# Kernel tuning notes

Measured on AMD Instinct MI355X. Metric: run time of the kernel, lower is better.

Reference implementation:

```python
import jax, jax.numpy as jnp
import numpy as np

N = 50000       # nodes
D_IN = 256      # in_channels
D_OUT = 256     # out_channels
E1 = 300000     # edges for TAGConv branch
E2 = 300000     # edges for attention branch


def setup_inputs() -> dict:
    key = jax.random.key(0)
    ks = jax.random.split(key, 8)
    s = 1.0 / np.sqrt(D_IN)  # torch Linear default init range
    u = lambda k: jax.random.uniform(k, (D_IN, D_OUT), jnp.float32, -s, s)
    return {
        "x": jax.random.normal(ks[0], (N, D_IN), jnp.float32),
        "edge_index": jax.random.randint(ks[1], (2, E1), 0, N),
        "edge_index_2": jax.random.randint(ks[2], (2, E2), 0, N),
        "W0": u(ks[3]),  # TAGConv hop-0 weight
        "W1": u(ks[4]),  # TAGConv hop-1 weight
        "Wq": u(ks[5]),  # attention query proj
        "Wk": u(ks[6]),  # attention key proj
        "Wv": u(ks[7]),  # attention value proj
    }


def reference(x, edge_index, edge_index_2, W0, W1, Wq, Wk, Wv):
    # --- TAGConv branch: K=1, normalize=False, bias=False ---
    src, dst = edge_index[0], edge_index[1]
    agg = jax.ops.segment_sum(x[src], dst, num_segments=N)   # A @ x, [N, D_IN]
    x1 = x @ W0 + agg @ W1                                   # [N, D_OUT]

    # --- Transformer_Block branch over edge_index_2, use_softmax=False ---
    q = x @ Wq
    k = x @ Wk
    v = x @ Wv
    s2, d2 = edge_index_2[0], edge_index_2[1]
    attn = jnp.einsum('ed,ed->e', q[d2], k[s2])              # per-edge raw score
    x2 = jax.ops.segment_sum(attn[:, None] * v[s2], d2, num_segments=N)

    return x1 - x2
```

## Files before the change

### kernel.cpp

```cpp
#include <hip/hip_runtime.h>

#define TD 256

typedef __attribute__((ext_vector_type(8))) short short8;
typedef __attribute__((ext_vector_type(8))) unsigned short ushort8;
typedef __attribute__((ext_vector_type(4))) float f32x4;

__device__ inline unsigned short f2bf(float f) {
  unsigned u = __float_as_uint(f);
  u = u + 0x7fffu + ((u >> 16) & 1u);
  return (unsigned short)(u >> 16);
}
__device__ inline float bf2f(unsigned short h) {
  return __uint_as_float(((unsigned)h) << 16);
}

__global__ __launch_bounds__(256) void prologue_kernel(
    const int* __restrict__ ei, int E1, const int* __restrict__ ei2, int E2,
    int* __restrict__ deg1, int* __restrict__ deg2,
    const float* __restrict__ x, unsigned short* __restrict__ xb, long total8,
    const float* __restrict__ Wq, const float* __restrict__ Wk,
    unsigned short* __restrict__ wqb, unsigned short* __restrict__ wkb,
    const float* __restrict__ W0, const float* __restrict__ W1,
    const float* __restrict__ Wv, unsigned short* __restrict__ wt,
    int nbH, int nbX) {
  int b = blockIdx.x;
  if (b < nbH) {
    int stride = nbH * 256;
    int Emax = max(E1, E2);
    for (int i = b * 256 + threadIdx.x; i < Emax; i += stride) {
      if (i < E1) atomicAdd(&deg1[ei[E1 + i]], 1);
      if (i < E2) atomicAdd(&deg2[ei2[E2 + i]], 1);
    }
  } else if (b < nbH + nbX) {
    long t = (long)(b - nbH) * 256 + threadIdx.x;
    if (t >= total8) return;
    const float4 f0 = *reinterpret_cast<const float4*>(x + t * 8);
    const float4 f1 = *reinterpret_cast<const float4*>(x + t * 8 + 4);
    ushort8 o;
    o[0] = f2bf(f0.x); o[1] = f2bf(f0.y); o[2] = f2bf(f0.z); o[3] = f2bf(f0.w);
    o[4] = f2bf(f1.x); o[5] = f2bf(f1.y); o[6] = f2bf(f1.z); o[7] = f2bf(f1.w);
    *reinterpret_cast<ushort8*>(xb + t * 8) = o;
  } else if (b < nbH + nbX + 64) {
    int t = (b - nbH - nbX) * 256 + threadIdx.x;
    const float* src = (t < 8192) ? Wq : Wk;
    unsigned short* dst = (t < 8192) ? wqb : wkb;
    int o = (t & 8191) * 8;
    ushort8 r;
#pragma unroll
    for (int j = 0; j < 8; j++) r[j] = f2bf(src[o + j]);
    *reinterpret_cast<ushort8*>(dst + o) = r;
  } else {
    int b2 = b - nbH - nbX - 64;
    int m = b2 >> 8;
    int n = b2 & 255;
    int k = threadIdx.x;
    const float* W = m == 0 ? W0 : m == 1 ? W1 : Wv;
    wt[m * 65536 + n * 256 + k] = f2bf(W[k * 256 + n]);
  }
}

__global__ __launch_bounds__(256) void scanA_gemmG_kernel(
    const int* __restrict__ deg1, const int* __restrict__ deg2, int N,
    int* __restrict__ bsum,
    const unsigned short* __restrict__ wqb, const unsigned short* __restrict__ wkb,
    unsigned short* __restrict__ gt) {
  if (blockIdx.x < 512) {
    int arr = blockIdx.x >> 8;
    int b = blockIdx.x & 255;
    const int* deg = arr ? deg2 : deg1;
    int i = b * 256 + threadIdx.x;
    int v = (i < N) ? deg[i] : 0;
#pragma unroll
    for (int m = 1; m < 64; m <<= 1) v += __shfl_xor(v, m, 64);
    __shared__ int wsum[4];
    if ((threadIdx.x & 63) == 0) wsum[threadIdx.x >> 6] = v;
    __syncthreads();
    if (threadIdx.x == 0)
      bsum[blockIdx.x] = wsum[0] + wsum[1] + wsum[2] + wsum[3];
    return;
  }
  const int t = (blockIdx.x - 512) * 4 + (threadIdx.x >> 6);
  const int l = threadIdx.x & 63;
  const int a0 = (t >> 2) * 64;
  const int b0 = (t & 3) * 64;
  const int lc = l & 15;
  const int lk = l >> 4;
  f32x4 acc[4][4] = {};
#pragma unroll
  for (int ks = 0; ks < 256; ks += 32) {
    const int ko = ks + lk * 8;
    short8 a[4], b[4];
#pragma unroll
    for (int m = 0; m < 4; m++)
      a[m] = *reinterpret_cast<const short8*>(wqb + (a0 + m * 16 + lc) * 256 + ko);
#pragma unroll
    for (int n = 0; n < 4; n++)
      b[n] = *reinterpret_cast<const short8*>(wkb + (b0 + n * 16 + lc) * 256 + ko);
#pragma unroll
    for (int m = 0; m < 4; m++)
#pragma unroll
      for (int n = 0; n < 4; n++)
        acc[m][n] =
            __builtin_amdgcn_mfma_f32_16x16x32_bf16(a[m], b[n], acc[m][n], 0, 0, 0);
  }
#pragma unroll
  for (int m = 0; m < 4; m++)
#pragma unroll
    for (int n = 0; n < 4; n++)
#pragma unroll
      for (int j = 0; j < 4; j++) {
        int a = a0 + m * 16 + lk * 4 + j;
        int b = b0 + n * 16 + lc;
        gt[b * 256 + a] = f2bf(acc[m][n][j]);
      }
}

__global__ __launch_bounds__(256) void scan_fill_kernel(
    const int* __restrict__ deg1, const int* __restrict__ deg2,
    const int* __restrict__ bsum, int N,
    int* __restrict__ off1, int* __restrict__ cur1,
    int* __restrict__ off2, int* __restrict__ cur2) {
  int arr = blockIdx.x >> 8;
  int b = blockIdx.x & 255;
  const int* deg = arr ? deg2 : deg1;
  int* off = arr ? off2 : off1;
  int* cur = arr ? cur2 : cur1;
  const int t = threadIdx.x;

  __shared__ int redp[4], redt[4];
  int sval = bsum[arr * 256 + t];
  int pv = (t < b) ? sval : 0;
  int tv = sval;
#pragma unroll
  for (int m = 1; m < 64; m <<= 1) {
    pv += __shfl_xor(pv, m, 64);
    tv += __shfl_xor(tv, m, 64);
  }
  if ((t & 63) == 0) { redp[t >> 6] = pv; redt[t >> 6] = tv; }
  __syncthreads();
  int prefix = redp[0] + redp[1] + redp[2] + redp[3];
  int total = redt[0] + redt[1] + redt[2] + redt[3];
  if (b == 255 && t == 0) off[N] = total;

  int i = b * 256 + t;
  __shared__ int sm[256];
  int v = (i < N) ? deg[i] : 0;
  sm[t] = v;
  __syncthreads();
  for (int d = 1; d < 256; d <<= 1) {
    int val = (t >= d) ? sm[t - d] : 0;
    __syncthreads();
    sm[t] += val;
    __syncthreads();
  }
  int e = sm[t] - v + prefix;
  if (i < N) {
    off[i] = e;
    cur[i] = e;
  }
}

__global__ __launch_bounds__(256) void fill_kernel(
    const int* __restrict__ ei, int E1, const int* __restrict__ ei2, int E2,
    int* __restrict__ cur1, int* __restrict__ cur2,
    int* __restrict__ csr1, int* __restrict__ csr2) {
  int stride = gridDim.x * blockDim.x;
  int Emax = max(E1, E2);
  for (int i = blockIdx.x * blockDim.x + threadIdx.x; i < Emax; i += stride) {
    if (i < E1) {
      int d = ei[E1 + i];
      int p = atomicAdd(&cur1[d], 1);
      csr1[p] = ei[i];
    }
    if (i < E2) {
      int d = ei2[E2 + i];
      int p = atomicAdd(&cur2[d], 1);
      csr2[p] = ei2[i];
    }
  }
}

__global__ __launch_bounds__(256) void gather_fused_kernel(
    const unsigned short* __restrict__ xb, const unsigned short* __restrict__ qb,
    const int* __restrict__ off1, const int* __restrict__ csr1,
    const int* __restrict__ off2, const int* __restrict__ csr2,
    int N, unsigned short* __restrict__ aggb, unsigned short* __restrict__ tb) {
  int wid = blockIdx.x * 4 + (threadIdx.x >> 6);
  if (wid >= N) return;
  int lane = threadIdx.x & 63;

  {
    int beg = off1[wid], end = off1[wid + 1];
    float ax = 0.f, ay = 0.f, az = 0.f, aw = 0.f;
    for (int j = beg; j < end; j += 4) {
      int e1 = end - 1;
      int s0 = csr1[j];
      int s1 = csr1[j + 1 < end ? j + 1 : e1];
      int s2 = csr1[j + 2 < end ? j + 2 : e1];
      int s3 = csr1[j + 3 < end ? j + 3 : e1];
      float m1 = (j + 1 < end) ? 1.f : 0.f;
      float m2 = (j + 2 < end) ? 1.f : 0.f;
      float m3 = (j + 3 < end) ? 1.f : 0.f;
      ushort4 r0 = *reinterpret_cast<const ushort4*>(xb + (size_t)s0 * TD + lane * 4);
      ushort4 r1 = *reinterpret_cast<const ushort4*>(xb + (size_t)s1 * TD + lane * 4);
      ushort4 r2 = *reinterpret_cast<const ushort4*>(xb + (size_t)s2 * TD + lane * 4);
      ushort4 r3 = *reinterpret_cast<const ushort4*>(xb + (size_t)s3 * TD + lane * 4);
      ax += bf2f(r0.x) + m1 * bf2f(r1.x) + m2 * bf2f(r2.x) + m3 * bf2f(r3.x);
      ay += bf2f(r0.y) + m1 * bf2f(r1.y) + m2 * bf2f(r2.y) + m3 * bf2f(r3.y);
      az += bf2f(r0.z) + m1 * bf2f(r1.z) + m2 * bf2f(r2.z) + m3 * bf2f(r3.z);
      aw += bf2f(r0.w) + m1 * bf2f(r1.w) + m2 * bf2f(r2.w) + m3 * bf2f(r3.w);
    }
    ushort4 o;
    o.x = f2bf(ax); o.y = f2bf(ay); o.z = f2bf(az); o.w = f2bf(aw);
    *reinterpret_cast<ushort4*>(aggb + (size_t)wid * TD + lane * 4) = o;
  }

  {
    ushort4 qv = *reinterpret_cast<const ushort4*>(qb + (size_t)wid * TD + lane * 4);
    float qx = bf2f(qv.x), qy = bf2f(qv.y), qz = bf2f(qv.z), qw = bf2f(qv.w);
    int beg = off2[wid], end = off2[wid + 1];
    float tx = 0.f, ty = 0.f, tz = 0.f, tw = 0.f;
    for (int j = beg; j < end; j += 4) {
      int e1 = end - 1;
      int s0 = csr2[j];
      int s1 = csr2[j + 1 < end ? j + 1 : e1];
      int s2 = csr2[j + 2 < end ? j + 2 : e1];
      int s3 = csr2[j + 3 < end ? j + 3 : e1];
      ushort4 r0 = *reinterpret_cast<const ushort4*>(xb + (size_t)s0 * TD + lane * 4);
      ushort4 r1 = *reinterpret_cast<const ushort4*>(xb + (size_t)s1 * TD + lane * 4);
      ushort4 r2 = *reinterpret_cast<const ushort4*>(xb + (size_t)s2 * TD + lane * 4);
      ushort4 r3 = *reinterpret_cast<const ushort4*>(xb + (size_t)s3 * TD + lane * 4);
      float a0x = bf2f(r0.x), a0y = bf2f(r0.y), a0z = bf2f(r0.z), a0w = bf2f(r0.w);
      float a1x = bf2f(r1.x), a1y = bf2f(r1.y), a1z = bf2f(r1.z), a1w = bf2f(r1.w);
      float a2x = bf2f(r2.x), a2y = bf2f(r2.y), a2z = bf2f(r2.z), a2w = bf2f(r2.w);
      float a3x = bf2f(r3.x), a3y = bf2f(r3.y), a3z = bf2f(r3.z), a3w = bf2f(r3.w);
      float p0 = qx * a0x + qy * a0y + qz * a0z + qw * a0w;
      float p1 = qx * a1x + qy * a1y + qz * a1z + qw * a1w;
      float p2 = qx * a2x + qy * a2y + qz * a2z + qw * a2w;
      float p3 = qx * a3x + qy * a3y + qz * a3z + qw * a3w;
#pragma unroll
      for (int m = 1; m < 64; m <<= 1) {
        p0 += __shfl_xor(p0, m, 64);
        p1 += __shfl_xor(p1, m, 64);
        p2 += __shfl_xor(p2, m, 64);
        p3 += __shfl_xor(p3, m, 64);
      }
      p1 = (j + 1 < end) ? p1 : 0.f;
      p2 = (j + 2 < end) ? p2 : 0.f;
      p3 = (j + 3 < end) ? p3 : 0.f;
      tx -= p0 * a0x + p1 * a1x + p2 * a2x + p3 * a3x;
      ty -= p0 * a0y + p1 * a1y + p2 * a2y + p3 * a3y;
      tz -= p0 * a0z + p1 * a1z + p2 * a2z + p3 * a3z;
      tw -= p0 * a0w + p1 * a1w + p2 * a2w + p3 * a3w;
    }
    ushort4 o;
    o.x = f2bf(tx); o.y = f2bf(ty); o.z = f2bf(tz); o.w = f2bf(tw);
    *reinterpret_cast<ushort4*>(tb + (size_t)wid * TD + lane * 4) = o;
  }
}

template <int MODE>
__global__ __launch_bounds__(512) void gemm_lds(
    const unsigned short* __restrict__ xb, const unsigned short* __restrict__ aggb,
    const unsigned short* __restrict__ tb, const unsigned short* __restrict__ wt,
    const unsigned short* __restrict__ gt, float* __restrict__ out,
    unsigned short* __restrict__ qb, int M) {
  __shared__ __align__(16) unsigned short sA[128 * 64];
  __shared__ __align__(16) unsigned short sB[256 * 64];

  const int m0 = blockIdx.x * 128;
  const int tid = threadIdx.x;
  const int w = tid >> 6, l = tid & 63;
  const int lrow = l >> 3, lslot = l & 7;
  const int wr = w >> 2, wc = w & 3;

  f32x4 acc[4][4] = {};

  const int KTOT = (MODE == 0) ? 256 : 768;

  for (int k0 = 0; k0 < KTOT; k0 += 64) {
    const unsigned short* Ap;
    const unsigned short* Bp;
    int ks;
    if (MODE == 0) {
      Ap = xb; Bp = gt; ks = k0;
    } else {
      int seg = k0 >> 8;
      Ap = seg == 0 ? xb : seg == 1 ? aggb : tb;
      Bp = wt + seg * 65536;
      ks = k0 & 255;
    }

#pragma unroll
    for (int i = 0; i < 2; i++) {
      int row = w * 16 + i * 8 + lrow;
      int gr = m0 + row;
      if (gr >= M) gr = M - 1;
      int g = lslot ^ lrow;
      const unsigned short* src = Ap + (size_t)gr * TD + ks + g * 8;
      unsigned short* dst = sA + (w * 16 + i * 8) * 64;
      __builtin_amdgcn_global_load_lds(
          (const __attribute__((address_space(1))) void*)src,
          (__attribute__((address_space(3))) void*)dst, 16, 0, 0);
    }
#pragma unroll
    for (int i = 0; i < 4; i++) {
      int row = w * 32 + i * 8 + lrow;
      int g = lslot ^ lrow;
      const unsigned short* src = Bp + (size_t)row * TD + ks + g * 8;
      unsigned short* dst = sB + (w * 32 + i * 8) * 64;
      __builtin_amdgcn_global_load_lds(
          (const __attribute__((address_space(1))) void*)src,
          (__attribute__((address_space(3))) void*)dst, 16, 0, 0);
    }
    __syncthreads();

#pragma unroll
    for (int kk = 0; kk < 2; kk++) {
      short8 a[4], b[4];
#pragma unroll
      for (int m = 0; m < 4; m++) {
        int row = wr * 64 + m * 16 + (l & 15);
        int slot = (kk * 4 + (l >> 4)) ^ (row & 7);
        a[m] = *reinterpret_cast<const short8*>(&sA[row * 64 + slot * 8]);
      }
#pragma unroll
      for (int n = 0; n < 4; n++) {
        int row = wc * 64 + n * 16 + (l & 15);
        int slot = (kk * 4 + (l >> 4)) ^ (row & 7);
        b[n] = *reinterpret_cast<const short8*>(&sB[row * 64 + slot * 8]);
      }
#pragma unroll
      for (int m = 0; m < 4; m++)
#pragma unroll
        for (int n = 0; n < 4; n++)
          acc[m][n] =
              __builtin_amdgcn_mfma_f32_16x16x32_bf16(a[m], b[n], acc[m][n], 0, 0, 0);
    }
    __syncthreads();
  }

  if (MODE == 1) {
#pragma unroll
    for (int m = 0; m < 4; m++)
#pragma unroll
      for (int n = 0; n < 4; n++)
#pragma unroll
        for (int j = 0; j < 4; j++) {
          int r = m0 + wr * 64 + m * 16 + (l >> 4) * 4 + j;
          if (r < M)
            out[(size_t)r * TD + wc * 64 + n * 16 + (l & 15)] = acc[m][n][j];
        }
  } else {
#pragma unroll
    for (int m = 0; m < 4; m++)
#pragma unroll
      for (int n = 0; n < 4; n++)
#pragma unroll
        for (int j = 0; j < 4; j++) {
          int r = m0 + wr * 64 + m * 16 + (l >> 4) * 4 + j;
          if (r < M)
            qb[(size_t)r * TD + wc * 64 + n * 16 + (l & 15)] =
                f2bf(acc[m][n][j]);
        }
  }
}

extern "C" void kernel_launch(void* const* d_in, const int* in_sizes, int n_in,
                              void* d_out, int out_size, void* d_ws,
                              size_t ws_size, hipStream_t stream) {
  const float* x  = (const float*)d_in[0];
  const int*   ei  = (const int*)d_in[1];
  const int*   ei2 = (const int*)d_in[2];
  const float* W0 = (const float*)d_in[3];
  const float* W1 = (const float*)d_in[4];
  const float* Wq = (const float*)d_in[5];
  const float* Wk = (const float*)d_in[6];
  const float* Wv = (const float*)d_in[7];

  const int N  = in_sizes[0] / TD;
  const int E1 = in_sizes[1] / 2;
  const int E2 = in_sizes[2] / 2;

  float* out = (float*)d_out;
  const size_t rowN = (size_t)N * TD;

  char* p = (char*)d_ws;
  unsigned short* xb   = (unsigned short*)p; p += rowN * 2;
  unsigned short* aggb = (unsigned short*)p; p += rowN * 2;
  unsigned short* qb   = (unsigned short*)p; p += rowN * 2;
  unsigned short* tb   = (unsigned short*)p; p += rowN * 2;
  unsigned short* wt   = (unsigned short*)p; p += 3 * 65536 * 2;
  unsigned short* gt   = (unsigned short*)p; p += 65536 * 2;
  unsigned short* wqb  = (unsigned short*)p; p += 65536 * 2;
  unsigned short* wkb  = (unsigned short*)p; p += 65536 * 2;
  int* off1 = (int*)p; p += (N + 1) * 4;
  int* cur1 = (int*)p; p += N * 4;
  int* off2 = (int*)p; p += (N + 1) * 4;
  int* cur2 = (int*)p; p += N * 4;
  int* csr1 = (int*)p; p += (size_t)E1 * 4;
  int* csr2 = (int*)p; p += (size_t)E2 * 4;
  int* deg1 = (int*)p; p += N * 4;
  int* deg2 = (int*)p; p += N * 4;
  int* bsum = (int*)p; p += 512 * 4;

  hipMemsetAsync(deg1, 0, (size_t)2 * N * sizeof(int), stream);

  long total8 = rowN / 8;
  int nbH = 512;
  int nbX = (int)((total8 + 255) / 256);
  prologue_kernel<<<nbH + nbX + 64 + 768, 256, 0, stream>>>(
      ei, E1, ei2, E2, deg1, deg2, x, xb, total8, Wq, Wk, wqb, wkb, W0, W1, Wv,
      wt, nbH, nbX);

  scanA_gemmG_kernel<<<516, 256, 0, stream>>>(deg1, deg2, N, bsum, wqb, wkb, gt);
  scan_fill_kernel<<<512, 256, 0, stream>>>(deg1, deg2, bsum, N, off1, cur1,
                                            off2, cur2);
  fill_kernel<<<1024, 256, 0, stream>>>(ei, E1, ei2, E2, cur1, cur2, csr1, csr2);

  int gblk = (N + 127) / 128;
  gemm_lds<0><<<gblk, 512, 0, stream>>>(xb, aggb, tb, wt, gt, out, qb, N);

  gather_fused_kernel<<<(N + 3) / 4, 256, 0, stream>>>(xb, qb, off1, csr1,
                                                       off2, csr2, N, aggb, tb);

  gemm_lds<1><<<gblk, 512, 0, stream>>>(xb, aggb, tb, wt, gt, out, qb, N);
}
```

Before: 183.0 us.

## Fuse CSR fill with first GEMM, double-buffer GEMM LDS, unroll gathers by eight

The CSR fill pass and the Q·K^T GEMM now run as one launch: the first FB blocks do the atomic fill and the remaining blocks do the GEMM, so the two independent jobs overlap and one launch is saved. Both GEMMs now use double-buffered LDS with a K step of 32, so the next tile is prefetched while MFMAs run on the current one, with a new 4-slot XOR swizzle. The gather loops for both branches are unrolled from 4 to 8 edges to put more loads in flight. The costs are higher register pressure in the gather, twice the barriers per unit of K in the GEMM, and a fixed FB split that may not balance the two kinds of work.

```diff
diff --git a/kernel.cpp b/kernel.cpp
--- a/kernel.cpp
+++ b/kernel.cpp
@@ -161,24 +161,159 @@
   }
 }
 
-__global__ __launch_bounds__(256) void fill_kernel(
+template <int MODE>
+__device__ __forceinline__ void stage_step(
+    const unsigned short* Ap, const unsigned short* Bp, int m0, int ks, int M,
+    int t, unsigned short* sAbuf, unsigned short* sBbuf) {
+  const int r = t >> 2, s = t & 3;
+  {
+    int g = (s ^ (r & 3) ^ ((r >> 2) & 3)) & 3;
+    int gr = m0 + r;
+    if (gr >= M) gr = M - 1;
+    __builtin_amdgcn_global_load_lds(
+        (const __attribute__((address_space(1))) void*)(Ap + (size_t)gr * TD + ks + g * 8),
+        (__attribute__((address_space(3))) void*)(sAbuf + r * 32 + s * 8), 16, 0, 0);
+  }
+#pragma unroll
+  for (int i = 0; i < 2; i++) {
+    int rb = r + i * 128;
+    int g = (s ^ (rb & 3) ^ ((rb >> 2) & 3)) & 3;
+    __builtin_amdgcn_global_load_lds(
+        (const __attribute__((address_space(1))) void*)(Bp + (size_t)rb * TD + ks + g * 8),
+        (__attribute__((address_space(3))) void*)(sBbuf + rb * 32 + s * 8), 16, 0, 0);
+  }
+}
+
+template <int MODE>
+__device__ __forceinline__ void gemm_body(
+    int bid, const unsigned short* __restrict__ xb,
+    const unsigned short* __restrict__ aggb, const unsigned short* __restrict__ tb,
+    const unsigned short* __restrict__ wt, const unsigned short* __restrict__ gt,
+    float* __restrict__ out, unsigned short* __restrict__ qb, int M,
+    unsigned short* sA, unsigned short* sB) {
+  const int m0 = bid * 128;
+  const int tid = threadIdx.x;
+  const int w = tid >> 6, l = tid & 63;
+  const int wr = w >> 2, wc = w & 3;
+
+  f32x4 acc[4][4] = {};
+
+  const int NSTEP = (MODE == 0) ? 8 : 24;
+
+  const unsigned short* Ap;
+  const unsigned short* Bp;
+  int ks;
+#define SRCS(step)                                                     \
+  {                                                                    \
+    int k0 = (step) * 32;                                              \
+    if (MODE == 0) { Ap = xb; Bp = gt; ks = k0; }                      \
+    else {                                                             \
+      int seg = k0 >> 8;                                               \
+      Ap = seg == 0 ? xb : seg == 1 ? aggb : tb;                       \
+      Bp = wt + seg * 65536;                                           \
+      ks = k0 & 255;                                                   \
+    }                                                                  \
+  }
+
+  SRCS(0);
+  stage_step<MODE>(Ap, Bp, m0, ks, M, tid, sA, sB);
+  __syncthreads();
+
+  int cur = 0;
+  for (int step = 0; step < NSTEP; ++step) {
+    if (step + 1 < NSTEP) {
+      SRCS(step + 1);
+      stage_step<MODE>(Ap, Bp, m0, ks, M, tid, sA + (cur ^ 1) * 4096,
+                       sB + (cur ^ 1) * 8192);
+    }
+    const unsigned short* cA = sA + cur * 4096;
+    const unsigned short* cB = sB + cur * 8192;
+    short8 a[4], b[4];
+#pragma unroll
+    for (int m = 0; m < 4; m++) {
+      int R = wr * 64 + m * 16 + (l & 15);
+      int slot = ((l >> 4) ^ (R & 3) ^ ((R >> 2) & 3)) & 3;
+      a[m] = *reinterpret_cast<const short8*>(&cA[R * 32 + slot * 8]);
+    }
+#pragma unroll
+    for (int n = 0; n < 4; n++) {
+      int R = wc * 64 + n * 16 + (l & 15);
+      int slot = ((l >> 4) ^ (R & 3) ^ ((R >> 2) & 3)) & 3;
+      b[n] = *reinterpret_cast<const short8*>(&cB[R * 32 + slot * 8]);
+    }
+#pragma unroll
+    for (int m = 0; m < 4; m++)
+#pragma unroll
+      for (int n = 0; n < 4; n++)
+        acc[m][n] =
+            __builtin_amdgcn_mfma_f32_16x16x32_bf16(a[m], b[n], acc[m][n], 0, 0, 0);
+    __syncthreads();
+    cur ^= 1;
+  }
+#undef SRCS
+
+  if (MODE == 1) {
+#pragma unroll
+    for (int m = 0; m < 4; m++)
+#pragma unroll
+      for (int n = 0; n < 4; n++)
+#pragma unroll
+        for (int j = 0; j < 4; j++) {
+          int r = m0 + wr * 64 + m * 16 + (l >> 4) * 4 + j;
+          if (r < M)
+            out[(size_t)r * TD + wc * 64 + n * 16 + (l & 15)] = acc[m][n][j];
+        }
+  } else {
+#pragma unroll
+    for (int m = 0; m < 4; m++)
+#pragma unroll
+      for (int n = 0; n < 4; n++)
+#pragma unroll
+        for (int j = 0; j < 4; j++) {
+          int r = m0 + wr * 64 + m * 16 + (l >> 4) * 4 + j;
+          if (r < M)
+            qb[(size_t)r * TD + wc * 64 + n * 16 + (l & 15)] =
+                f2bf(acc[m][n][j]);
+        }
+  }
+}
+
+__global__ __launch_bounds__(512) void fill_gemm0_kernel(
     const int* __restrict__ ei, int E1, const int* __restrict__ ei2, int E2,
     int* __restrict__ cur1, int* __restrict__ cur2,
-    int* __restrict__ csr1, int* __restrict__ csr2) {
-  int stride = gridDim.x * blockDim.x;
-  int Emax = max(E1, E2);
-  for (int i = blockIdx.x * blockDim.x + threadIdx.x; i < Emax; i += stride) {
-    if (i < E1) {
-      int d = ei[E1 + i];
-      int p = atomicAdd(&cur1[d], 1);
-      csr1[p] = ei[i];
-    }
-    if (i < E2) {
-      int d = ei2[E2 + i];
-      int p = atomicAdd(&cur2[d], 1);
-      csr2[p] = ei2[i];
-    }
-  }
+    int* __restrict__ csr1, int* __restrict__ csr2,
+    const unsigned short* __restrict__ xb, const unsigned short* __restrict__ gt,
+    unsigned short* __restrict__ qb, int M, int FB) {
+  __shared__ __align__(16) unsigned short sA[2 * 128 * 32];
+  __shared__ __align__(16) unsigned short sB[2 * 256 * 32];
+  if (blockIdx.x < FB) {
+    int stride = FB * 512;
+    int Emax = max(E1, E2);
+    for (int i = blockIdx.x * 512 + threadIdx.x; i < Emax; i += stride) {
+      if (i < E1) {
+        int d = ei[E1 + i];
+        int p = atomicAdd(&cur1[d], 1);
+        csr1[p] = ei[i];
+      }
+      if (i < E2) {
+        int d = ei2[E2 + i];
+        int p = atomicAdd(&cur2[d], 1);
+        csr2[p] = ei2[i];
+      }
+    }
+    return;
+  }
+  gemm_body<0>(blockIdx.x - FB, xb, nullptr, nullptr, nullptr, gt, nullptr, qb,
+               M, sA, sB);
+}
+
+__global__ __launch_bounds__(512) void gemm1_kernel(
+    const unsigned short* __restrict__ xb, const unsigned short* __restrict__ aggb,
+    const unsigned short* __restrict__ tb, const unsigned short* __restrict__ wt,
+    float* __restrict__ out, int M) {
+  __shared__ __align__(16) unsigned short sA[2 * 128 * 32];
+  __shared__ __align__(16) unsigned short sB[2 * 256 * 32];
+  gemm_body<1>(blockIdx.x, xb, aggb, tb, wt, nullptr, out, nullptr, M, sA, sB);
 }
 
 __global__ __launch_bounds__(256) void gather_fused_kernel(
@@ -193,23 +328,24 @@
   {
     int beg = off1[wid], end = off1[wid + 1];
     float ax = 0.f, ay = 0.f, az = 0.f, aw = 0.f;
-    for (int j = beg; j < end; j += 4) {
+    for (int j = beg; j < end; j += 8) {
       int e1 = end - 1;
-      int s0 = csr1[j];
-      int s1 = csr1[j + 1 < end ? j + 1 : e1];
-      int s2 = csr1[j + 2 < end ? j + 2 : e1];
-      int s3 = csr1[j + 3 < end ? j + 3 : e1];
-      float m1 = (j + 1 < end) ? 1.f : 0.f;
-      float m2 = (j + 2 < end) ? 1.f : 0.f;
-      float m3 = (j + 3 < end) ? 1.f : 0.f;
-      ushort4 r0 = *reinterpret_cast<const ushort4*>(xb + (size_t)s0 * TD + lane * 4);
-      ushort4 r1 = *reinterpret_cast<const ushort4*>(xb + (size_t)s1 * TD + lane * 4);
-      ushort4 r2 = *reinterpret_cast<const ushort4*>(xb + (size_t)s2 * TD + lane * 4);
-      ushort4 r3 = *reinterpret_cast<const ushort4*>(xb + (size_t)s3 * TD + lane * 4);
-      ax += bf2f(r0.x) + m1 * bf2f(r1.x) + m2 * bf2f(r2.x) + m3 * bf2f(r3.x);
-      ay += bf2f(r0.y) + m1 * bf2f(r1.y) + m2 * bf2f(r2.y) + m3 * bf2f(r3.y);
-      az += bf2f(r0.z) + m1 * bf2f(r1.z) + m2 * bf2f(r2.z) + m3 * bf2f(r3.z);
-      aw += bf2f(r0.w) + m1 * bf2f(r1.w) + m2 * bf2f(r2.w) + m3 * bf2f(r3.w);
+      ushort4 r[8];
+      float mk[8];
+#pragma unroll
+      for (int i = 0; i < 8; i++) {
+        int jj = j + i;
+        int s = csr1[jj < end ? jj : e1];
+        mk[i] = (jj < end) ? 1.f : 0.f;
+        r[i] = *reinterpret_cast<const ushort4*>(xb + (size_t)s * TD + lane * 4);
+      }
+#pragma unroll
+      for (int i = 0; i < 8; i++) {
+        ax += mk[i] * bf2f(r[i].x);
+        ay += mk[i] * bf2f(r[i].y);
+        az += mk[i] * bf2f(r[i].z);
+        aw += mk[i] * bf2f(r[i].w);
+      }
     }
     ushort4 o;
     o.x = f2bf(ax); o.y = f2bf(ay); o.z = f2bf(az); o.w = f2bf(aw);
@@ -221,149 +357,37 @@
     float qx = bf2f(qv.x), qy = bf2f(qv.y), qz = bf2f(qv.z), qw = bf2f(qv.w);
     int beg = off2[wid], end = off2[wid + 1];
     float tx = 0.f, ty = 0.f, tz = 0.f, tw = 0.f;
-    for (int j = beg; j < end; j += 4) {
+    for (int j = beg; j < end; j += 8) {
       int e1 = end - 1;
-      int s0 = csr2[j];
-      int s1 = csr2[j + 1 < end ? j + 1 : e1];
-      int s2 = csr2[j + 2 < end ? j + 2 : e1];
-      int s3 = csr2[j + 3 < end ? j + 3 : e1];
-      ushort4 r0 = *reinterpret_cast<const ushort4*>(xb + (size_t)s0 * TD + lane * 4);
-      ushort4 r1 = *reinterpret_cast<const ushort4*>(xb + (size_t)s1 * TD + lane * 4);
-      ushort4 r2 = *reinterpret_cast<const ushort4*>(xb + (size_t)s2 * TD + lane * 4);
-      ushort4 r3 = *reinterpret_cast<const ushort4*>(xb + (size_t)s3 * TD + lane * 4);
-      float a0x = bf2f(r0.x), a0y = bf2f(r0.y), a0z = bf2f(r0.z), a0w = bf2f(r0.w);
-      float a1x = bf2f(r1.x), a1y = bf2f(r1.y), a1z = bf2f(r1.z), a1w = bf2f(r1.w);
-      float a2x = bf2f(r2.x), a2y = bf2f(r2.y), a2z = bf2f(r2.z), a2w = bf2f(r2.w);
-      float a3x = bf2f(r3.x), a3y = bf2f(r3.y), a3z = bf2f(r3.z), a3w = bf2f(r3.w);
-      float p0 = qx * a0x + qy * a0y + qz * a0z + qw * a0w;
-      float p1 = qx * a1x + qy * a1y + qz * a1z + qw * a1w;
-      float p2 = qx * a2x + qy * a2y + qz * a2z + qw * a2w;
-      float p3 = qx * a3x + qy * a3y + qz * a3z + qw * a3w;
+      float vx[8][4];
+      float px[8];
+#pragma unroll
+      for (int i = 0; i < 8; i++) {
+        int jj = j + i;
+        int s = csr2[jj < end ? jj : e1];
+        ushort4 r = *reinterpret_cast<const ushort4*>(xb + (size_t)s * TD + lane * 4);
+        vx[i][0] = bf2f(r.x); vx[i][1] = bf2f(r.y);
+        vx[i][2] = bf2f(r.z); vx[i][3] = bf2f(r.w);
+        px[i] = qx * vx[i][0] + qy * vx[i][1] + qz * vx[i][2] + qw * vx[i][3];
+      }
 #pragma unroll
       for (int m = 1; m < 64; m <<= 1) {
-        p0 += __shfl_xor(p0, m, 64);
-        p1 += __shfl_xor(p1, m, 64);
-        p2 += __shfl_xor(p2, m, 64);
-        p3 += __shfl_xor(p3, m, 64);
-      }
-      p1 = (j + 1 < end) ? p1 : 0.f;
-      p2 = (j + 2 < end) ? p2 : 0.f;
-      p3 = (j + 3 < end) ? p3 : 0.f;
-      tx -= p0 * a0x + p1 * a1x + p2 * a2x + p3 * a3x;
-      ty -= p0 * a0y + p1 * a1y + p2 * a2y + p3 * a3y;
-      tz -= p0 * a0z + p1 * a1z + p2 * a2z + p3 * a3z;
-      tw -= p0 * a0w + p1 * a1w + p2 * a2w + p3 * a3w;
+#pragma unroll
+        for (int i = 0; i < 8; i++) px[i] += __shfl_xor(px[i], m, 64);
+      }
+#pragma unroll
+      for (int i = 1; i < 8; i++) px[i] = (j + i < end) ? px[i] : 0.f;
+#pragma unroll
+      for (int i = 0; i < 8; i++) {
+        tx -= px[i] * vx[i][0];
+        ty -= px[i] * vx[i][1];
+        tz -= px[i] * vx[i][2];
+        tw -= px[i] * vx[i][3];
+      }
     }
     ushort4 o;
     o.x = f2bf(tx); o.y = f2bf(ty); o.z = f2bf(tz); o.w = f2bf(tw);
     *reinterpret_cast<ushort4*>(tb + (size_t)wid * TD + lane * 4) = o;
-  }
-}
-
-template <int MODE>
-__global__ __launch_bounds__(512) void gemm_lds(
-    const unsigned short* __restrict__ xb, const unsigned short* __restrict__ aggb,
-    const unsigned short* __restrict__ tb, const unsigned short* __restrict__ wt,
-    const unsigned short* __restrict__ gt, float* __restrict__ out,
-    unsigned short* __restrict__ qb, int M) {
-  __shared__ __align__(16) unsigned short sA[128 * 64];
-  __shared__ __align__(16) unsigned short sB[256 * 64];
-
-  const int m0 = blockIdx.x * 128;
-  const int tid = threadIdx.x;
-  const int w = tid >> 6, l = tid & 63;
-  const int lrow = l >> 3, lslot = l & 7;
-  const int wr = w >> 2, wc = w & 3;
-
-  f32x4 acc[4][4] = {};
-
-  const int KTOT = (MODE == 0) ? 256 : 768;
-
-  for (int k0 = 0; k0 < KTOT; k0 += 64) {
-    const unsigned short* Ap;
-    const unsigned short* Bp;
-    int ks;
-    if (MODE == 0) {
-      Ap = xb; Bp = gt; ks = k0;
-    } else {
-      int seg = k0 >> 8;
-      Ap = seg == 0 ? xb : seg == 1 ? aggb : tb;
-      Bp = wt + seg * 65536;
-      ks = k0 & 255;
-    }
-
-#pragma unroll
-    for (int i = 0; i < 2; i++) {
-      int row = w * 16 + i * 8 + lrow;
-      int gr = m0 + row;
-      if (gr >= M) gr = M - 1;
-      int g = lslot ^ lrow;
-      const unsigned short* src = Ap + (size_t)gr * TD + ks + g * 8;
-      unsigned short* dst = sA + (w * 16 + i * 8) * 64;
-      __builtin_amdgcn_global_load_lds(
-          (const __attribute__((address_space(1))) void*)src,
-          (__attribute__((address_space(3))) void*)dst, 16, 0, 0);
-    }
-#pragma unroll
-    for (int i = 0; i < 4; i++) {
-      int row = w * 32 + i * 8 + lrow;
-      int g = lslot ^ lrow;
-      const unsigned short* src = Bp + (size_t)row * TD + ks + g * 8;
-      unsigned short* dst = sB + (w * 32 + i * 8) * 64;
-      __builtin_amdgcn_global_load_lds(
-          (const __attribute__((address_space(1))) void*)src,
-          (__attribute__((address_space(3))) void*)dst, 16, 0, 0);
-    }
-    __syncthreads();
-
-#pragma unroll
-    for (int kk = 0; kk < 2; kk++) {
-      short8 a[4], b[4];
-#pragma unroll
-      for (int m = 0; m < 4; m++) {
-        int row = wr * 64 + m * 16 + (l & 15);
-        int slot = (kk * 4 + (l >> 4)) ^ (row & 7);
-        a[m] = *reinterpret_cast<const short8*>(&sA[row * 64 + slot * 8]);
-      }
-#pragma unroll
-      for (int n = 0; n < 4; n++) {
-        int row = wc * 64 + n * 16 + (l & 15);
-        int slot = (kk * 4 + (l >> 4)) ^ (row & 7);
-        b[n] = *reinterpret_cast<const short8*>(&sB[row * 64 + slot * 8]);
-      }
-#pragma unroll
-      for (int m = 0; m < 4; m++)
-#pragma unroll
-        for (int n = 0; n < 4; n++)
-          acc[m][n] =
-              __builtin_amdgcn_mfma_f32_16x16x32_bf16(a[m], b[n], acc[m][n], 0, 0, 0);
-    }
-    __syncthreads();
-  }
-
-  if (MODE == 1) {
-#pragma unroll
-    for (int m = 0; m < 4; m++)
-#pragma unroll
-      for (int n = 0; n < 4; n++)
-#pragma unroll
-        for (int j = 0; j < 4; j++) {
-          int r = m0 + wr * 64 + m * 16 + (l >> 4) * 4 + j;
-          if (r < M)
-            out[(size_t)r * TD + wc * 64 + n * 16 + (l & 15)] = acc[m][n][j];
-        }
-  } else {
-#pragma unroll
-    for (int m = 0; m < 4; m++)
-#pragma unroll
-      for (int n = 0; n < 4; n++)
-#pragma unroll
-        for (int j = 0; j < 4; j++) {
-          int r = m0 + wr * 64 + m * 16 + (l >> 4) * 4 + j;
-          if (r < M)
-            qb[(size_t)r * TD + wc * 64 + n * 16 + (l & 15)] =
-                f2bf(acc[m][n][j]);
-        }
   }
 }
 
@@ -417,13 +441,14 @@
   scanA_gemmG_kernel<<<516, 256, 0, stream>>>(deg1, deg2, N, bsum, wqb, wkb, gt);
   scan_fill_kernel<<<512, 256, 0, stream>>>(deg1, deg2, bsum, N, off1, cur1,
                                             off2, cur2);
-  fill_kernel<<<1024, 256, 0, stream>>>(ei, E1, ei2, E2, cur1, cur2, csr1, csr2);
 
   int gblk = (N + 127) / 128;
-  gemm_lds<0><<<gblk, 512, 0, stream>>>(xb, aggb, tb, wt, gt, out, qb, N);
+  int FB = 384;
+  fill_gemm0_kernel<<<FB + gblk, 512, 0, stream>>>(
+      ei, E1, ei2, E2, cur1, cur2, csr1, csr2, xb, gt, qb, N, FB);
 
   gather_fused_kernel<<<(N + 3) / 4, 256, 0, stream>>>(xb, qb, off1, csr1,
                                                        off2, csr2, N, aggb, tb);
 
-  gemm_lds<1><<<gblk, 512, 0, stream>>>(xb, aggb, tb, wt, gt, out, qb, N);
-}
+  gemm1_kernel<<<gblk, 512, 0, stream>>>(xb, aggb, tb, wt, out, N);
+}
```

After: 200.5 us. +9.5%, slower.
